# Performance work log

Measured on AMD Instinct MI355X. Metric: run time of the kernel, lower is better.

## Reference

```python
import jax, jax.numpy as jnp
import numpy as np

B, S, D, P, NQ = 8, 2048, 1024, 256, 8192


def setup_inputs() -> dict:
    key = jax.random.key(0)
    ks = jax.random.split(key, 8)
    return {
        "flag": 0,
        "encoded_input": jax.random.normal(ks[0], (B, S, D), dtype=jnp.float32),
        "start_ids_1": jax.random.randint(ks[1], (NQ,), 0, S, dtype=jnp.int32),
        "end_ids_1": jax.random.randint(ks[2], (NQ,), 0, S, dtype=jnp.int32),
        "query_batch_idx": jax.random.randint(ks[3], (NQ,), 0, B, dtype=jnp.int32),
        "start_ids_2": jax.random.randint(ks[4], (NQ,), 0, S, dtype=jnp.int32),
        "end_ids_2": jax.random.randint(ks[5], (NQ,), 0, S, dtype=jnp.int32),
        "W": jax.random.normal(ks[6], (D, P), dtype=jnp.float32) * 0.02,
        "b": jnp.zeros((P,), dtype=jnp.float32),
    }


def _gather_spans(h, qb, s, e):
    # span_repr[b, i, j] = concat(h[b, i], h[b, j]) for j >= i, else 0.
    # Direct gather instead of building the O(seq^2) table.
    rep = jnp.concatenate([h[qb, s], h[qb, e]], axis=-1)  # [NQ, 2*P]
    valid = (e >= s).astype(rep.dtype)[:, None]
    return rep * valid


def reference(flag, encoded_input, start_ids_1, end_ids_1, query_batch_idx,
              start_ids_2, end_ids_2, W, b):
    h = encoded_input @ W + b  # [B, S, P] (use_proj=True)
    res1 = _gather_spans(h, query_batch_idx, start_ids_1, end_ids_1)
    res2 = _gather_spans(h, query_batch_idx, start_ids_2, end_ids_2)
    return (res1, res2)
```

## Files before the change

### kernel.cpp

```cpp
#include <hip/hip_runtime.h>
#include <hip/hip_bf16.h>
#include <stdint.h>

#define S_LEN 2048
#define D_DIM 1024
#define P_DIM 256
#define NQ_   8192
#define M_TOT 16384

typedef __attribute__((ext_vector_type(4))) float  f32x4;
typedef __attribute__((ext_vector_type(8))) __bf16 bf16x8;
typedef __attribute__((ext_vector_type(4))) __bf16 bf16x4;

__global__ __launch_bounds__(1024) void wt_kernel(const float* __restrict__ W,
                                                  __bf16* __restrict__ WT) {
    __shared__ __bf16 tile[32][33];
    const int k0 = blockIdx.x * 32;
    const int n0 = blockIdx.y * 32;
    const int tx = threadIdx.x, ty = threadIdx.y;
    tile[ty][tx] = (__bf16)W[(k0 + ty) * P_DIM + (n0 + tx)];
    __syncthreads();
    WT[(n0 + ty) * D_DIM + (k0 + tx)] = tile[tx][ty];
}

__global__ __launch_bounds__(256) void gemm_kernel(const float*  __restrict__ A,
                                                   const __bf16* __restrict__ WT,
                                                   const float*  __restrict__ bias,
                                                   float*        __restrict__ H) {
    __shared__ __bf16 As[64 * 32];
    __shared__ __bf16 Bs[256 * 32];

    const int tid = threadIdx.x;
    const int w   = tid >> 6;
    const int l   = tid & 63;
    const int lm  = l & 15;
    const int q   = l >> 4;

    const int m0 = blockIdx.x * 64;

    f32x4 acc[4][4] = {};

    for (int k0 = 0; k0 < D_DIM; k0 += 32) {
        #pragma unroll
        for (int i = 0; i < 2; ++i) {
            const int ch  = tid + i * 256;
            const int row = ch >> 3;
            const int c4  = (ch & 7) << 2;
            const float4 va = *(const float4*)(A + (size_t)(m0 + row) * D_DIM + k0 + c4);
            bf16x4 vb;
            vb[0] = (__bf16)va.x; vb[1] = (__bf16)va.y;
            vb[2] = (__bf16)va.z; vb[3] = (__bf16)va.w;
            *(bf16x4*)(As + row * 32 + c4) = vb;
        }
        #pragma unroll
        for (int i = 0; i < 4; ++i) {
            const int ch = tid + i * 256;
            const int n  = ch >> 2;
            const int c8 = (ch & 3) << 3;
            *(uint4*)(Bs + n * 32 + c8) =
                *(const uint4*)(WT + (size_t)n * D_DIM + k0 + c8);
        }
        __syncthreads();

        bf16x8 af[4], bfr[4];
        #pragma unroll
        for (int mi = 0; mi < 4; ++mi)
            af[mi] = *(const bf16x8*)(As + (mi * 16 + lm) * 32 + q * 8);
        #pragma unroll
        for (int ni = 0; ni < 4; ++ni)
            bfr[ni] = *(const bf16x8*)(Bs + (w * 64 + ni * 16 + lm) * 32 + q * 8);

        #pragma unroll
        for (int mi = 0; mi < 4; ++mi)
            #pragma unroll
            for (int ni = 0; ni < 4; ++ni)
                acc[mi][ni] = __builtin_amdgcn_mfma_f32_16x16x32_bf16(
                    af[mi], bfr[ni], acc[mi][ni], 0, 0, 0);

        __syncthreads();
    }

    #pragma unroll
    for (int ni = 0; ni < 4; ++ni) {
        const int col = w * 64 + ni * 16 + lm;
        const float bv = bias[col];
        #pragma unroll
        for (int mi = 0; mi < 4; ++mi) {
            #pragma unroll
            for (int r = 0; r < 4; ++r) {
                const int row = m0 + mi * 16 + q * 4 + r;
                H[(size_t)row * P_DIM + col] = acc[mi][ni][r] + bv;
            }
        }
    }
}

__global__ __launch_bounds__(256) void gather_kernel(const float* __restrict__ H,
                                                     const int* __restrict__ s1,
                                                     const int* __restrict__ e1,
                                                     const int* __restrict__ qb,
                                                     const int* __restrict__ s2,
                                                     const int* __restrict__ e2,
                                                     float* __restrict__ out) {
    const int qi  = blockIdx.x;
    const int t   = threadIdx.x;
    const int b   = qb[qi];
    const int set = t >> 7;
    const int rem = t & 127;
    const int half = rem >> 6;
    const int c4  = (rem & 63) << 2;

    const int s = set ? s2[qi] : s1[qi];
    const int e = set ? e2[qi] : e1[qi];

    float4 v = make_float4(0.f, 0.f, 0.f, 0.f);
    if (e >= s) {
        const int ridx = half ? e : s;
        v = *(const float4*)(H + ((size_t)b * S_LEN + ridx) * P_DIM + c4);
    }
    *(float4*)(out + (size_t)set * (NQ_ * 512) + (size_t)qi * 512 + half * 256 + c4) = v;
}

extern "C" void kernel_launch(void* const* d_in, const int* in_sizes, int n_in,
                              void* d_out, int out_size, void* d_ws, size_t ws_size,
                              hipStream_t stream) {
    const float* A    = (const float*)d_in[1];
    const int*   s1   = (const int*)  d_in[2];
    const int*   e1   = (const int*)  d_in[3];
    const int*   qb   = (const int*)  d_in[4];
    const int*   s2   = (const int*)  d_in[5];
    const int*   e2   = (const int*)  d_in[6];
    const float* W    = (const float*)d_in[7];
    const float* bias = (const float*)d_in[8];
    float*       out  = (float*)d_out;

    __bf16* WT = (__bf16*)d_ws;
    float*  H  = (float*)((char*)d_ws + (1 << 20));

    wt_kernel    <<<dim3(32, 8), dim3(32, 32), 0, stream>>>(W, WT);
    gemm_kernel  <<<dim3(M_TOT / 64), dim3(256), 0, stream>>>(A, WT, bias, H);
    gather_kernel<<<dim3(NQ_), dim3(256), 0, stream>>>(H, s1, e1, qb, s2, e2, out);
}
```

Baseline: 160.8 us.

## Replace LDS-staged GEMM with register-direct loads and software prefetch

The GEMM no longer stages A and W tiles through shared memory with barriers. Each lane loads its MFMA fragments straight from global memory into registers, prefetching the next K step while the current one computes. The M tile is halved to 32 rows, doubling the grid to 512 blocks. This removes LDS traffic and __syncthreads stalls, but A rows are now read redundantly by all four waves and each lane issues strided, less-coalesced global loads.

```diff
diff --git a/kernel.cpp b/kernel.cpp
--- a/kernel.cpp
+++ b/kernel.cpp
@@ -27,57 +27,80 @@
                                                    const __bf16* __restrict__ WT,
                                                    const float*  __restrict__ bias,
                                                    float*        __restrict__ H) {
-    __shared__ __bf16 As[64 * 32];
-    __shared__ __bf16 Bs[256 * 32];
-
     const int tid = threadIdx.x;
     const int w   = tid >> 6;
     const int l   = tid & 63;
     const int lm  = l & 15;
     const int q   = l >> 4;
 
-    const int m0 = blockIdx.x * 64;
+    const int m0 = blockIdx.x * 32;
 
-    f32x4 acc[4][4] = {};
+    const float*  pa = A  + (size_t)(m0 + lm) * D_DIM + q * 8;
+    const __bf16* pb = WT + (size_t)(w * 64 + lm) * D_DIM + q * 8;
 
-    for (int k0 = 0; k0 < D_DIM; k0 += 32) {
+    f32x4 acc[2][4] = {};
+
+    float4 ra[2][2];
+    bf16x8 rb[4];
+
+    #pragma unroll
+    for (int mi = 0; mi < 2; ++mi) {
+        ra[mi][0] = *(const float4*)(pa + mi * 16 * D_DIM);
+        ra[mi][1] = *(const float4*)(pa + mi * 16 * D_DIM + 4);
+    }
+    #pragma unroll
+    for (int ni = 0; ni < 4; ++ni)
+        rb[ni] = *(const bf16x8*)(pb + ni * 16 * D_DIM);
+
+    #pragma unroll 4
+    for (int k0 = 0; k0 < D_DIM - 32; k0 += 32) {
+        const int kn = k0 + 32;
+        float4 na[2][2];
+        bf16x8 nb[4];
         #pragma unroll
-        for (int i = 0; i < 2; ++i) {
-            const int ch  = tid + i * 256;
-            const int row = ch >> 3;
-            const int c4  = (ch & 7) << 2;
-            const float4 va = *(const float4*)(A + (size_t)(m0 + row) * D_DIM + k0 + c4);
-            bf16x4 vb;
-            vb[0] = (__bf16)va.x; vb[1] = (__bf16)va.y;
-            vb[2] = (__bf16)va.z; vb[3] = (__bf16)va.w;
-            *(bf16x4*)(As + row * 32 + c4) = vb;
+        for (int mi = 0; mi < 2; ++mi) {
+            na[mi][0] = *(const float4*)(pa + mi * 16 * D_DIM + kn);
+            na[mi][1] = *(const float4*)(pa + mi * 16 * D_DIM + kn + 4);
         }
         #pragma unroll
-        for (int i = 0; i < 4; ++i) {
-            const int ch = tid + i * 256;
-            const int n  = ch >> 2;
-            const int c8 = (ch & 3) << 3;
-            *(uint4*)(Bs + n * 32 + c8) =
-                *(const uint4*)(WT + (size_t)n * D_DIM + k0 + c8);
+        for (int ni = 0; ni < 4; ++ni)
+            nb[ni] = *(const bf16x8*)(pb + ni * 16 * D_DIM + kn);
+
+        bf16x8 af[2];
+        #pragma unroll
+        for (int mi = 0; mi < 2; ++mi) {
+            af[mi][0] = (__bf16)ra[mi][0].x; af[mi][1] = (__bf16)ra[mi][0].y;
+            af[mi][2] = (__bf16)ra[mi][0].z; af[mi][3] = (__bf16)ra[mi][0].w;
+            af[mi][4] = (__bf16)ra[mi][1].x; af[mi][5] = (__bf16)ra[mi][1].y;
+            af[mi][6] = (__bf16)ra[mi][1].z; af[mi][7] = (__bf16)ra[mi][1].w;
         }
-        __syncthreads();
-
-        bf16x8 af[4], bfr[4];
         #pragma unroll
-        for (int mi = 0; mi < 4; ++mi)
-            af[mi] = *(const bf16x8*)(As + (mi * 16 + lm) * 32 + q * 8);
-        #pragma unroll
-        for (int ni = 0; ni < 4; ++ni)
-            bfr[ni] = *(const bf16x8*)(Bs + (w * 64 + ni * 16 + lm) * 32 + q * 8);
-
-        #pragma unroll
-        for (int mi = 0; mi < 4; ++mi)
+        for (int mi = 0; mi < 2; ++mi)
             #pragma unroll
             for (int ni = 0; ni < 4; ++ni)
                 acc[mi][ni] = __builtin_amdgcn_mfma_f32_16x16x32_bf16(
-                    af[mi], bfr[ni], acc[mi][ni], 0, 0, 0);
+                    af[mi], rb[ni], acc[mi][ni], 0, 0, 0);
+        #pragma unroll
+        for (int mi = 0; mi < 2; ++mi) { ra[mi][0] = na[mi][0]; ra[mi][1] = na[mi][1]; }
+        #pragma unroll
+        for (int ni = 0; ni < 4; ++ni) rb[ni] = nb[ni];
+    }
 
-        __syncthreads();
+    {
+        bf16x8 af[2];
+        #pragma unroll
+        for (int mi = 0; mi < 2; ++mi) {
+            af[mi][0] = (__bf16)ra[mi][0].x; af[mi][1] = (__bf16)ra[mi][0].y;
+            af[mi][2] = (__bf16)ra[mi][0].z; af[mi][3] = (__bf16)ra[mi][0].w;
+            af[mi][4] = (__bf16)ra[mi][1].x; af[mi][5] = (__bf16)ra[mi][1].y;
+            af[mi][6] = (__bf16)ra[mi][1].z; af[mi][7] = (__bf16)ra[mi][1].w;
+        }
+        #pragma unroll
+        for (int mi = 0; mi < 2; ++mi)
+            #pragma unroll
+            for (int ni = 0; ni < 4; ++ni)
+                acc[mi][ni] = __builtin_amdgcn_mfma_f32_16x16x32_bf16(
+                    af[mi], rb[ni], acc[mi][ni], 0, 0, 0);
     }
 
     #pragma unroll
@@ -85,12 +108,11 @@
         const int col = w * 64 + ni * 16 + lm;
         const float bv = bias[col];
         #pragma unroll
-        for (int mi = 0; mi < 4; ++mi) {
+        for (int mi = 0; mi < 2; ++mi) {
+            const int rbase = m0 + mi * 16 + q * 4;
             #pragma unroll
-            for (int r = 0; r < 4; ++r) {
-                const int row = m0 + mi * 16 + q * 4 + r;
-                H[(size_t)row * P_DIM + col] = acc[mi][ni][r] + bv;
-            }
+            for (int r = 0; r < 4; ++r)
+                H[(size_t)(rbase + r) * P_DIM + col] = acc[mi][ni][r] + bv;
         }
     }
 }
@@ -138,6 +160,6 @@
     float*  H  = (float*)((char*)d_ws + (1 << 20));
 
     wt_kernel    <<<dim3(32, 8), dim3(32, 32), 0, stream>>>(W, WT);
-    gemm_kernel  <<<dim3(M_TOT / 64), dim3(256), 0, stream>>>(A, WT, bias, H);
+    gemm_kernel  <<<dim3(M_TOT / 32), dim3(256), 0, stream>>>(A, WT, bias, H);
     gather_kernel<<<dim3(NQ_), dim3(256), 0, stream>>>(H, s1, e1, qb, s2, e2, out);
 }
```

New measurement: 179.8 us. 11.8% more time.
